# Performance work log

Measured on AMD Instinct MI355X. Metric: run time of the kernel, lower is better.

Reference implementation:

```python
import jax, jax.numpy as jnp
import numpy as np

B, T, I, H, O = 64, 256, 128, 512, 64
GRAD_CLIP = 5.0


def setup_inputs() -> dict:
    key = jax.random.key(0)
    ks = jax.random.split(key, 20)
    sH = 1.0 / np.sqrt(H)
    sI = 1.0 / np.sqrt(I)
    f32 = jnp.float32
    return {
        "x": jax.random.normal(ks[0], (B, T, I), f32),
        "y": jax.random.randint(ks[1], (B,), 0, O),
        "W1w": jax.random.normal(ks[2], (H, H), f32) * sH,
        "V1w": jax.random.normal(ks[3], (H, I), f32) * sI,
        "V1b": jnp.zeros((H,), f32),
        "W2w": jax.random.normal(ks[4], (H, H), f32) * sH,
        "W2b": jnp.zeros((H,), f32),
        "V2w": jax.random.normal(ks[5], (H, I), f32) * sI,
        "W3w": jax.random.normal(ks[6], (H, H), f32) * sH,
        "W3b": jnp.zeros((H,), f32),
        "V3w": jax.random.normal(ks[7], (H, I), f32) * sI,
        "Woutw": jax.random.normal(ks[8], (O, H), f32) * sH,
        "Woutb": jnp.zeros((O,), f32),
        "BW1": jax.random.normal(ks[9], (O, H), f32) * sH,
        "BV1": jax.random.normal(ks[10], (O, H), f32) * sH,
        "BW2": jax.random.normal(ks[11], (O, H), f32) * sH,
        "BV2": jax.random.normal(ks[12], (O, H), f32) * sH,
        "BW3": jax.random.normal(ks[13], (O, H), f32) * sH,
        "BV3": jax.random.normal(ks[14], (O, H), f32) * sH,
    }


def reference(x, y, W1w, V1w, V1b, W2w, W2b, V2w, W3w, W3b, V3w,
              Woutw, Woutb, BW1, BV1, BW2, BV2, BW3, BV3):
    Bsz, Tlen, _ = x.shape
    Hd = W1w.shape[0]
    Od = Woutw.shape[0]
    h0 = jnp.zeros((Bsz, Hd), x.dtype)
    xt = jnp.swapaxes(x, 0, 1)  # [T, B, I]

    def step(h, xti):
        z = jax.nn.sigmoid(h @ W2w.T + W2b + xti @ V2w.T)
        r = jax.nn.sigmoid(h @ W3w.T + W3b + xti @ V3w.T)
        ht = jnp.tanh(xti @ V1w.T + V1b + (h * r) @ W1w.T)
        hn = (1.0 - z) * ht + z * h
        return hn, (r, z, ht, hn)

    hT, (rs, zs, hs, hid) = jax.lax.scan(step, h0, xt)  # each [T, B, H]
    output = jax.nn.softmax(hT @ Woutw.T + Woutb, axis=-1)
    error = output - jax.nn.one_hot(y, Od, dtype=output.dtype)

    BW1e, BV1e = error @ BW1, error @ BV1
    BW2e, BV2e = error @ BW2, error @ BV2
    BW3e, BV3e = error @ BW3, error @ BV3

    hiddens = jnp.concatenate([h0[None], hid], axis=0)  # [T+1, B, H]
    # Faithfully replicate torch's hiddens[t-1] list indexing: at t=0 this is
    # hiddens[-1], i.e. the FINAL hidden state (Python negative indexing).
    idx = (np.arange(Tlen) - 1) % (Tlen + 1)
    hprev = hiddens[idx]  # [T, B, H]

    rr = rs * (1.0 - rs)
    sz = 1.0 - zs
    dh = 1.0 - hs ** 2

    # z-gate terms (index 1) -- original code uses r*(1-r) here, replicated.
    zg = (hprev - hs) * rr
    zgV = zg * BV2e[None]
    zgW = zg * BW2e[None]
    dV1 = jnp.einsum('tbh,tbi->hi', zgV, xt) / Bsz
    dW1 = jnp.einsum('tbh,tbH->hH', zgW, hprev) / Bsz
    db1 = zgV.sum(0).mean(0)

    # r-gate terms (index 2)
    AV = ((BV3e[None] * sz * dh) @ W1w.T) * hprev * rr
    AW = ((BW3e[None] * sz * dh) @ W1w.T) * hprev * rr
    dV2 = jnp.einsum('tbh,tbi->hi', AV, xt) / Bsz
    dW2 = jnp.einsum('tbh,tbH->hH', AW, hprev) / Bsz
    db2 = AV.sum(0).mean(0)

    # h-gate terms (index 0)
    HV = ((BV1e[None] * sz) @ W1w.T) * dh
    HW = ((BW1e[None] * sz) @ W1w.T) * dh
    dV0 = jnp.einsum('tbh,tbi->hi', HV, xt) / Bsz
    dW0 = jnp.einsum('tbh,tbH->hH', HW, rs * hprev) / Bsz
    db0 = HV.sum(0).mean(0)

    def nc(g):
        g = g / jnp.linalg.norm(g)
        return jnp.clip(g, -GRAD_CLIP, GRAD_CLIP)

    return (output, hT,
            nc(dW0), nc(dW1), nc(dW2),
            nc(dV0), nc(dV1), nc(dV2),
            nc(db0), nc(db1), nc(db2),
            error)
```

## Files before the change

kernel.cpp:

```cpp
#include <hip/hip_runtime.h>
#include <hip/hip_bf16.h>

#define DI __device__ __forceinline__

typedef __bf16 bf16x8 __attribute__((ext_vector_type(8)));
typedef __bf16 bf16x4 __attribute__((ext_vector_type(4)));
typedef __bf16 bf16x2 __attribute__((ext_vector_type(2)));
typedef float  f32x4  __attribute__((ext_vector_type(4)));
typedef unsigned long long ull;

static constexpr int Bc = 64, Tc = 256, Ic = 128, Hc = 512, Oc = 64;
static constexpr int TBc = Tc * Bc;
static constexpr size_t THW = (size_t)TBc * Hc;

static constexpr size_t O_OUT = 0;
static constexpr size_t O_HT  = 4096;
static constexpr size_t O_DW0 = 36864;
static constexpr size_t O_DV0 = 823296;
static constexpr size_t O_DB0 = 1019904;
static constexpr size_t O_ERR = 1021440;

static constexpr size_t W_CTR  = 0;
static constexpr size_t W_SLOT = 1024;
static constexpr size_t W_DB   = 2048;
static constexpr size_t W_FLG  = 8192;
static constexpr size_t W_ERRW = 16384;
static constexpr size_t W_PROJ = 32768;
static constexpr size_t W_W1B  = 819200;
static constexpr size_t W_HX   = 1343488;
static constexpr size_t W_HRX  = 1474560;
static constexpr size_t W_XT   = 1605632;
static constexpr size_t W_HIST = 5799936;
static constexpr size_t W_PB   = 72908800;
static constexpr size_t W_NEED = W_PB + 100663296;


DI void st32_agent(float* p, float v) {
  __hip_atomic_store((unsigned int*)p, __float_as_uint(v),
                     __ATOMIC_RELAXED, __HIP_MEMORY_SCOPE_AGENT);
}
DI ull ld64_agent(const void* p) {
  return __hip_atomic_load((ull*)p, __ATOMIC_RELAXED, __HIP_MEMORY_SCOPE_AGENT);
}

DI void group_barrier(int* flags_g, int myslot, int bar, bool& dead) {
  __syncthreads();
  if (threadIdx.x == 0)
    __hip_atomic_store(&flags_g[myslot * 32], bar,
                       __ATOMIC_RELAXED, __HIP_MEMORY_SCOPE_AGENT);
  if (threadIdx.x < 64 && !dead) {
    const int l = threadIdx.x;
    int spins = 0;
    for (;;) {
      int v = bar;
      if (l < 16)
        v = __hip_atomic_load(&flags_g[l * 32],
                              __ATOMIC_RELAXED, __HIP_MEMORY_SCOPE_AGENT);
      if (__all(v >= bar)) break;
      __builtin_amdgcn_s_sleep(1);
      if (++spins > 4000000) { dead = true; break; }
    }
  }
  __syncthreads();
}

DI float hprev_at(const __bf16* __restrict__ h_h, int k, int col) {
  int t = k >> 6;
  if (t == 1) return 0.f;
  int row = (t == 0) ? (16320 + (k & 63)) : (k - 128);
  return (float)h_h[(size_t)row * 512 + col];
}


__global__ void kzero(float* __restrict__ p, int n) {
  int i = blockIdx.x * 256 + threadIdx.x;
  if (i < n) p[i] = 0.f;
}
__global__ void ksent(float* p, float v) { p[0] = v; }
__global__ void k0_cast(const float* __restrict__ s, __bf16* __restrict__ d, int n) {
  int i = blockIdx.x * 256 + threadIdx.x;
  if (i < n) d[i] = (__bf16)s[i];
}

__global__ __launch_bounds__(256)
void k1_xv(const float* __restrict__ x, const float* __restrict__ V1w,
           const float* __restrict__ V2w, const float* __restrict__ V3w,
           const float* __restrict__ V1b, const float* __restrict__ W2b,
           const float* __restrict__ W3b,
           float* __restrict__ xv1f, float* __restrict__ xv2f, float* __restrict__ xv3f)
{
  const int cb = blockIdx.x, t = blockIdx.y;
  const int g = cb >> 3, jblk = cb & 7;
  const float* Vg   = (g == 0) ? V1w : (g == 1) ? V2w : V3w;
  const float* bias = (g == 0) ? V1b : (g == 1) ? W2b : W3b;
  float* of = (g == 0) ? xv1f : (g == 1) ? xv2f : xv3f;
  __shared__ float As[64 * 69];
  __shared__ float Bs[64 * 69];
  const int tid = threadIdx.x;
  float acc[4][4] = {};
  const int m0 = (tid & 15) * 4, j0 = (tid >> 4) * 4;
  for (int kc = 0; kc < 2; ++kc) {
    __syncthreads();
    #pragma unroll
    for (int e = 0; e < 4; ++e) {
      int idx = tid + e * 256;
      int row = idx >> 4, c4 = (idx & 15) * 4;
      float4 v = *reinterpret_cast<const float4*>(&x[((size_t)row * 256 + t) * 128 + kc * 64 + c4]);
      As[row * 69 + c4 + 0] = v.x; As[row * 69 + c4 + 1] = v.y;
      As[row * 69 + c4 + 2] = v.z; As[row * 69 + c4 + 3] = v.w;
      float4 w = *reinterpret_cast<const float4*>(&Vg[(size_t)(jblk * 64 + row) * 128 + kc * 64 + c4]);
      Bs[row * 69 + c4 + 0] = w.x; Bs[row * 69 + c4 + 1] = w.y;
      Bs[row * 69 + c4 + 2] = w.z; Bs[row * 69 + c4 + 3] = w.w;
    }
    __syncthreads();
    for (int i = 0; i < 64; ++i) {
      float a[4], b[4];
      #pragma unroll
      for (int u = 0; u < 4; ++u) a[u] = As[(m0 + u) * 69 + i];
      #pragma unroll
      for (int u = 0; u < 4; ++u) b[u] = Bs[(j0 + u) * 69 + i];
      #pragma unroll
      for (int mi = 0; mi < 4; ++mi)
        #pragma unroll
        for (int ji = 0; ji < 4; ++ji) acc[mi][ji] += a[mi] * b[ji];
    }
  }
  #pragma unroll
  for (int ji = 0; ji < 4; ++ji) {
    int jg = jblk * 64 + j0 + ji;
    float bv = bias[jg];
    #pragma unroll
    for (int mi = 0; mi < 4; ++mi) {
      int b = m0 + mi;
      of[((size_t)t * 64 + b) * 512 + jg] = acc[mi][ji] + bv;
    }
  }
}

__global__ void e0_xt(const float* __restrict__ x, __bf16* __restrict__ XT)
{
  const int t = blockIdx.x;
  __shared__ __bf16 xs[64 * 132];
  const int tid = threadIdx.x;
  #pragma unroll
  for (int e = 0; e < 8; ++e) {
    int idx = tid + e * 256;
    int b = idx >> 5, c4 = (idx & 31) * 4;
    float4 v = *reinterpret_cast<const float4*>(&x[((size_t)b * 256 + t) * 128 + c4]);
    xs[b * 132 + c4 + 0] = (__bf16)v.x; xs[b * 132 + c4 + 1] = (__bf16)v.y;
    xs[b * 132 + c4 + 2] = (__bf16)v.z; xs[b * 132 + c4 + 3] = (__bf16)v.w;
  }
  __syncthreads();
  #pragma unroll
  for (int e = 0; e < 8; ++e) {
    int idx = tid + e * 256;
    int i = idx >> 4, b4 = (idx & 15) * 4;
    __bf16* d = &XT[(size_t)i * TBc + t * 64 + b4];
    d[0] = xs[(b4 + 0) * 132 + i];
    d[1] = xs[(b4 + 1) * 132 + i];
    d[2] = xs[(b4 + 2) * 132 + i];
    d[3] = xs[(b4 + 3) * 132 + i];
  }
}

__global__ __launch_bounds__(256, 1)
void k2_recur(const float* __restrict__ W1w, const float* __restrict__ W2w,
              const float* __restrict__ W3w,
              const float* __restrict__ xv1, const float* __restrict__ xv2,
              const float* __restrict__ xv3,
              __bf16* __restrict__ r_h, __bf16* __restrict__ z_h,
              __bf16* __restrict__ ht_h, __bf16* __restrict__ h_h,
              float* __restrict__ hx, float* __restrict__ hrx,
              int* __restrict__ flags, float* __restrict__ dout)
{
  const int g  = blockIdx.x >> 4;
  const int cw = blockIdx.x & 15;
  const int tid = threadIdx.x, lane = tid & 63, wv = tid >> 6;
  const int kh = wv & 1;
  const int ct = wv >> 1;
  const int q  = lane >> 4;
  const int colc = cw * 32 + ct * 16 + (lane & 15);
  const bool owner = (kh == 0);

  __shared__ __align__(16) __bf16 c0[8192];
  __shared__ __align__(16) __bf16 c1[8192];
  __shared__ __align__(16) __bf16 c2[8192];
  __shared__ float pbuf[128 * 8];

  bf16x8 w1c[3][8], w2c[3][8], w3c[3][8];
  #pragma unroll
  for (int kk2 = 0; kk2 < 8; ++kk2) {
    const int kb = (kh * 8 + kk2) * 32 + q * 8;
    #pragma unroll
    for (int j = 0; j < 8; ++j) {
      float w = W1w[(size_t)colc * 512 + kb + j];
      __bf16 a = (__bf16)w; float r1 = w - (float)a;
      __bf16 b = (__bf16)r1;
      w1c[0][kk2][j] = a; w1c[1][kk2][j] = b; w1c[2][kk2][j] = (__bf16)(r1 - (float)b);
      w = W2w[(size_t)colc * 512 + kb + j];
      a = (__bf16)w; r1 = w - (float)a; b = (__bf16)r1;
      w2c[0][kk2][j] = a; w2c[1][kk2][j] = b; w2c[2][kk2][j] = (__bf16)(r1 - (float)b);
      w = W3w[(size_t)colc * 512 + kb + j];
      a = (__bf16)w; r1 = w - (float)a; b = (__bf16)r1;
      w3c[0][kk2][j] = a; w3c[1][kk2][j] = b; w3c[2][kk2][j] = (__bf16)(r1 - (float)b);
    }
  }
  for (int i = tid; i < 8192; i += 256) {
    c0[i] = (__bf16)0.f; c1[i] = (__bf16)0.f; c2[i] = (__bf16)0.f;
  }
  __syncthreads();

  float hreg[4] = {0.f, 0.f, 0.f, 0.f};
  float* hx_g  = hx  + g * 8192;
  float* hrx_g = hrx + g * 8192;
  int* flags_g = flags + g * 16 * 32;
  const int fragbase = (colc >> 5) * 512 + (((colc >> 3) & 3) * 16 + q * 4) * 8 + (colc & 7);
  const int pb = (ct * 64 + lane) * 8;

  auto stage = [&](const float* __restrict__ srcf) {
    const ull* src = reinterpret_cast<const ull*>(srcf);
    ull u[16];
    #pragma unroll
    for (int j = 0; j < 16; ++j) u[j] = ld64_agent(src + j * 256 + tid);
    #pragma unroll
    for (int j = 0; j < 16; ++j) {
      float f0 = __uint_as_float((unsigned int)u[j]);
      float f1 = __uint_as_float((unsigned int)(u[j] >> 32));
      __bf16 a0 = (__bf16)f0; float r0 = f0 - (float)a0; __bf16 b0 = (__bf16)r0;
      __bf16 d0 = (__bf16)(r0 - (float)b0);
      __bf16 a1 = (__bf16)f1; float r1 = f1 - (float)a1; __bf16 b1 = (__bf16)r1;
      __bf16 d1 = (__bf16)(r1 - (float)b1);
      int o = (j * 256 + tid) * 2;
      bf16x2 v0; v0[0] = a0; v0[1] = a1;
      bf16x2 v1; v1[0] = b0; v1[1] = b1;
      bf16x2 v2; v2[0] = d0; v2[1] = d1;
      *reinterpret_cast<bf16x2*>(&c0[o]) = v0;
      *reinterpret_cast<bf16x2*>(&c1[o]) = v1;
      *reinterpret_cast<bf16x2*>(&c2[o]) = v2;
    }
  };

  bool dead = false;
  int bar = 0;
  #pragma unroll 1
  for (int t = 0; t < Tc; ++t) {
    const size_t rowb = ((size_t)t * 64 + g * 16 + q * 4) * 512 + colc;
    float xv1v[4], xv2v[4], xv3v[4];
    if (owner) {
      #pragma unroll
      for (int i = 0; i < 4; ++i) {
        size_t o = rowb + (size_t)i * 512;
        xv1v[i] = xv1[o]; xv2v[i] = xv2[o]; xv3v[i] = xv3[o];
      }
    }
    f32x4 a2 = {0.f,0.f,0.f,0.f}, a3 = {0.f,0.f,0.f,0.f};
    #pragma unroll
    for (int kk2 = 0; kk2 < 8; ++kk2) {
      const int idx = (kh * 8 + kk2) * 512 + lane * 8;
      bf16x8 h0 = *reinterpret_cast<const bf16x8*>(&c0[idx]);
      bf16x8 h1 = *reinterpret_cast<const bf16x8*>(&c1[idx]);
      bf16x8 h2 = *reinterpret_cast<const bf16x8*>(&c2[idx]);
      a2 = __builtin_amdgcn_mfma_f32_16x16x32_bf16(h0, w2c[0][kk2], a2, 0, 0, 0);
      a2 = __builtin_amdgcn_mfma_f32_16x16x32_bf16(h1, w2c[0][kk2], a2, 0, 0, 0);
      a2 = __builtin_amdgcn_mfma_f32_16x16x32_bf16(h0, w2c[1][kk2], a2, 0, 0, 0);
      a2 = __builtin_amdgcn_mfma_f32_16x16x32_bf16(h2, w2c[0][kk2], a2, 0, 0, 0);
      a2 = __builtin_amdgcn_mfma_f32_16x16x32_bf16(h1, w2c[1][kk2], a2, 0, 0, 0);
      a2 = __builtin_amdgcn_mfma_f32_16x16x32_bf16(h0, w2c[2][kk2], a2, 0, 0, 0);
      a3 = __builtin_amdgcn_mfma_f32_16x16x32_bf16(h0, w3c[0][kk2], a3, 0, 0, 0);
      a3 = __builtin_amdgcn_mfma_f32_16x16x32_bf16(h1, w3c[0][kk2], a3, 0, 0, 0);
      a3 = __builtin_amdgcn_mfma_f32_16x16x32_bf16(h0, w3c[1][kk2], a3, 0, 0, 0);
      a3 = __builtin_amdgcn_mfma_f32_16x16x32_bf16(h2, w3c[0][kk2], a3, 0, 0, 0);
      a3 = __builtin_amdgcn_mfma_f32_16x16x32_bf16(h1, w3c[1][kk2], a3, 0, 0, 0);
      a3 = __builtin_amdgcn_mfma_f32_16x16x32_bf16(h0, w3c[2][kk2], a3, 0, 0, 0);
    }
    if (!owner) {
      #pragma unroll
      for (int i = 0; i < 4; ++i) { pbuf[pb + i] = a2[i]; pbuf[pb + 4 + i] = a3[i]; }
    }
    __syncthreads();
    float zz[4], rr4[4];
    if (owner) {
      #pragma unroll
      for (int i = 0; i < 4; ++i) {
        float s2 = a2[i] + pbuf[pb + i]     + xv2v[i];
        float s3 = a3[i] + pbuf[pb + 4 + i] + xv3v[i];
        zz[i]  = 1.f / (1.f + expf(-s2));
        rr4[i] = 1.f / (1.f + expf(-s3));
        st32_agent(&hrx_g[fragbase + i * 8], hreg[i] * rr4[i]);
      }
      #pragma unroll
      for (int i = 0; i < 4; ++i) {
        z_h[rowb + (size_t)i * 512] = (__bf16)zz[i];
        r_h[rowb + (size_t)i * 512] = (__bf16)rr4[i];
      }
    }
    ++bar; group_barrier(flags_g, cw, bar, dead);
    stage(hrx_g);
    __syncthreads();
    f32x4 a1 = {0.f,0.f,0.f,0.f};
    #pragma unroll
    for (int kk2 = 0; kk2 < 8; ++kk2) {
      const int idx = (kh * 8 + kk2) * 512 + lane * 8;
      bf16x8 h0 = *reinterpret_cast<const bf16x8*>(&c0[idx]);
      bf16x8 h1 = *reinterpret_cast<const bf16x8*>(&c1[idx]);
      bf16x8 h2 = *reinterpret_cast<const bf16x8*>(&c2[idx]);
      a1 = __builtin_amdgcn_mfma_f32_16x16x32_bf16(h0, w1c[0][kk2], a1, 0, 0, 0);
      a1 = __builtin_amdgcn_mfma_f32_16x16x32_bf16(h1, w1c[0][kk2], a1, 0, 0, 0);
      a1 = __builtin_amdgcn_mfma_f32_16x16x32_bf16(h0, w1c[1][kk2], a1, 0, 0, 0);
      a1 = __builtin_amdgcn_mfma_f32_16x16x32_bf16(h2, w1c[0][kk2], a1, 0, 0, 0);
      a1 = __builtin_amdgcn_mfma_f32_16x16x32_bf16(h1, w1c[1][kk2], a1, 0, 0, 0);
      a1 = __builtin_amdgcn_mfma_f32_16x16x32_bf16(h0, w1c[2][kk2], a1, 0, 0, 0);
    }
    if (!owner) {
      #pragma unroll
      for (int i = 0; i < 4; ++i) pbuf[pb + i] = a1[i];
    }
    __syncthreads();
    if (owner) {
      float htv[4];
      #pragma unroll
      for (int i = 0; i < 4; ++i) {
        float pre = a1[i] + pbuf[pb + i] + xv1v[i];
        float ht = tanhf(pre);
        float hn = zz[i] * (hreg[i] - ht) + ht;
        htv[i] = ht;
        hreg[i] = hn;
        st32_agent(&hx_g[fragbase + i * 8], hn);
      }
      #pragma unroll
      for (int i = 0; i < 4; ++i) {
        ht_h[rowb + (size_t)i * 512] = (__bf16)htv[i];
        h_h[rowb + (size_t)i * 512]  = (__bf16)hreg[i];
      }
    }
    ++bar; group_barrier(flags_g, cw, bar, dead);
    stage(hx_g);
    __syncthreads();
  }
  if (owner) {
    #pragma unroll
    for (int i = 0; i < 4; ++i) {
      int b = g * 16 + q * 4 + i;
      dout[O_HT + (size_t)b * 512 + colc] = hreg[i];
    }
  }
}

__global__ void k3a_soft(const float* __restrict__ Woutw, const float* __restrict__ Woutb,
                         const int* __restrict__ y, float* __restrict__ dout,
                         float* __restrict__ errw)
{
  const int b = blockIdx.x, o = threadIdx.x;
  const float* hrow = dout + O_HT + (size_t)b * 512;
  float sv = Woutb[o];
  for (int k = 0; k < 512; ++k) sv += hrow[k] * Woutw[(size_t)o * 512 + k];
  float mx = sv;
  for (int off = 32; off; off >>= 1) mx = fmaxf(mx, __shfl_xor(mx, off, 64));
  float e = expf(sv - mx);
  float sum = e;
  for (int off = 32; off; off >>= 1) sum += __shfl_xor(sum, off, 64);
  float outp = e / sum;
  float errv = outp - ((y[b] == o) ? 1.f : 0.f);
  dout[O_OUT + b * 64 + o] = outp;
  dout[O_ERR + b * 64 + o] = errv;
  errw[b * 64 + o] = errv;
}

__global__ __launch_bounds__(256)
void k3b_proj(const float* __restrict__ err,
              const float* b0, const float* b1, const float* b2,
              const float* b3, const float* b4, const float* b5,
              float* __restrict__ proj)
{
  const int p = blockIdx.y;
  const int hb = blockIdx.x * 64;
  const float* BX = (p==0)?b0:(p==1)?b1:(p==2)?b2:(p==3)?b3:(p==4)?b4:b5;
  __shared__ float es[64 * 64];
  __shared__ float bs[64 * 65];
  for (int i = threadIdx.x; i < 4096; i += 256) es[i] = err[i];
  for (int i = threadIdx.x; i < 4096; i += 256) {
    int o = i >> 6, hh = i & 63;
    bs[o * 65 + hh] = BX[(size_t)o * 512 + hb + hh];
  }
  __syncthreads();
  for (int e = 0; e < 16; ++e) {
    int idx = threadIdx.x + e * 256;
    int b = idx >> 6, hh = idx & 63;
    float s = 0.f;
    for (int o = 0; o < 64; ++o) s += es[b * 64 + o] * bs[o * 65 + hh];
    proj[(size_t)p * 32768 + b * 512 + hb + hh] = s;
  }
}

__global__ __launch_bounds__(256)
void e1t(const __bf16* __restrict__ r_h, const __bf16* __restrict__ h_h,
         __bf16* __restrict__ HpT, __bf16* __restrict__ RsHpT)
{
  const int t = blockIdx.y, hb = blockIdx.x * 64;
  const int tid = threadIdx.x;
  __shared__ __bf16 tr[64 * 68];
  float hpv[16], rv[16];
  #pragma unroll
  for (int e = 0; e < 16; ++e) {
    int idx = tid + e * 256;
    int b = idx >> 6, hl = idx & 63;
    hpv[e] = hprev_at(h_h, t * 64 + b, hb + hl);
    rv[e]  = (float)r_h[((size_t)t * 64 + b) * 512 + hb + hl];
  }
  for (int rnd = 0; rnd < 2; ++rnd) {
    __syncthreads();
    #pragma unroll
    for (int e = 0; e < 16; ++e) {
      int idx = tid + e * 256;
      int b = idx >> 6, hl = idx & 63;
      tr[b * 68 + hl] = (__bf16)(rnd == 0 ? hpv[e] : rv[e] * hpv[e]);
    }
    __syncthreads();
    __bf16* dst = (rnd == 0) ? HpT : RsHpT;
    #pragma unroll
    for (int e = 0; e < 16; ++e) {
      int idx = tid + e * 256;
      int hl2 = idx >> 6, b2 = idx & 63;
      dst[(size_t)(hb + hl2) * TBc + t * 64 + b2] = tr[b2 * 68 + hl2];
    }
  }
}

__global__ __launch_bounds__(256)
void k4_pgemm(const __bf16* __restrict__ z_h, const __bf16* __restrict__ ht_h,
              const __bf16* __restrict__ r_h, const __bf16* __restrict__ h_h,
              const float* __restrict__ proj, const __bf16* __restrict__ W1b,
              __bf16* __restrict__ P)
{
  const int p = blockIdx.z;
  const int krow0 = blockIdx.x * 128;
  const int n0 = blockIdx.y * 128;
  const int pidx = (p == 0) ? 5 : (p == 1) ? 4 : (p == 2) ? 1 : 0;
  const float* pr = proj + (size_t)pidx * 32768;
  const int tid = threadIdx.x, lane = tid & 63, wv = tid >> 6, q = lane >> 4;
  const int wm = (wv & 1) * 64, wn = (wv >> 1) * 64;
  __shared__ __align__(16) __bf16 Al[128 * 40];
  __shared__ __align__(16) __bf16 Bl[128 * 40];
  f32x4 acc[4][4] = {};
  for (int kt = 0; kt < 16; ++kt) {
    const int h0 = kt * 32;
    __syncthreads();
    #pragma unroll
    for (int e = 0; e < 4; ++e) {
      int idx = tid + e * 256;
      int row = idx >> 3, h4 = (idx & 7) * 4;
      int kg = krow0 + row;
      bf16x4 zz = *reinterpret_cast<const bf16x4*>(&z_h[(size_t)kg * 512 + h0 + h4]);
      bf16x4 tt = *reinterpret_cast<const bf16x4*>(&ht_h[(size_t)kg * 512 + h0 + h4]);
      float4 pv = *reinterpret_cast<const float4*>(&pr[(size_t)(kg & 63) * 512 + h0 + h4]);
      float pvv[4] = {pv.x, pv.y, pv.z, pv.w};
      bf16x4 gv;
      #pragma unroll
      for (int j = 0; j < 4; ++j) {
        float sz = 1.f - (float)zz[j];
        float v = pvv[j] * sz;
        if (p < 2) { float h = (float)tt[j]; v *= (1.f - h * h); }
        gv[j] = (__bf16)v;
      }
      *reinterpret_cast<bf16x4*>(&Al[row * 40 + h4]) = gv;
      bf16x4 wv4 = *reinterpret_cast<const bf16x4*>(&W1b[(size_t)(n0 + row) * 512 + h0 + h4]);
      *reinterpret_cast<bf16x4*>(&Bl[row * 40 + h4]) = wv4;
    }
    __syncthreads();
    bf16x8 af[4], bfv[4];
    #pragma unroll
    for (int mi = 0; mi < 4; ++mi)
      af[mi] = *reinterpret_cast<const bf16x8*>(&Al[(wm + mi * 16 + (lane & 15)) * 40 + q * 8]);
    #pragma unroll
    for (int ni = 0; ni < 4; ++ni)
      bfv[ni] = *reinterpret_cast<const bf16x8*>(&Bl[(wn + ni * 16 + (lane & 15)) * 40 + q * 8]);
    #pragma unroll
    for (int mi = 0; mi < 4; ++mi)
      #pragma unroll
      for (int ni = 0; ni < 4; ++ni)
        acc[mi][ni] = __builtin_amdgcn_mfma_f32_16x16x32_bf16(af[mi], bfv[ni], acc[mi][ni], 0, 0, 0);
  }
  __bf16* Pp = P + (size_t)p * THW;
  #pragma unroll
  for (int mi = 0; mi < 4; ++mi) {
    const int kg = krow0 + wm + mi * 16 + q * 4;
    const int tt = kg >> 6;
    #pragma unroll
    for (int ni = 0; ni < 4; ++ni) {
      const int n = n0 + wn + ni * 16 + (lane & 15);
      union { __bf16 b[4]; uint2 u; } pk;
      #pragma unroll
      for (int i = 0; i < 4; ++i) {
        float mul;
        if (p < 2) {
          float r = (float)r_h[(size_t)(kg + i) * 512 + n];
          float hp = 0.f;
          if (tt != 1) {
            int kr = (tt == 0) ? (16320 + (kg & 63) + i) : (kg + i - 128);
            hp = (float)h_h[(size_t)kr * 512 + n];
          }
          mul = hp * r * (1.f - r);
        } else {
          float h = (float)ht_h[(size_t)(kg + i) * 512 + n];
          mul = 1.f - h * h;
        }
        pk.b[i] = (__bf16)(acc[mi][ni][i] * mul);
      }
      *reinterpret_cast<uint2*>(&Pp[(size_t)n * TBc + kg]) = pk.u;
    }
  }
}

__global__ __launch_bounds__(256)
void k5_grad(const __bf16* __restrict__ Ap, int amode, const __bf16* __restrict__ Bp,
             const __bf16* __restrict__ r_h, const __bf16* __restrict__ ht_h,
             const __bf16* __restrict__ h_h, const float* __restrict__ projA,
             float* __restrict__ out, int N, int klen, float scale)
{
  const int m0 = blockIdx.x * 128;
  const int n0 = blockIdx.y * 128;
  const int tid = threadIdx.x, lane = tid & 63, wv = tid >> 6, q = lane >> 4;
  const int wm = (wv & 1) * 64, wn = (wv >> 1) * 64;
  __shared__ __align__(16) __bf16 Al[128 * 72];
  __shared__ __align__(16) __bf16 Bl[128 * 72];
  f32x4 acc[4][4] = {};
  const int iters = klen >> 6;
  for (int kt = 0; kt < iters; ++kt) {
    const int kk0 = blockIdx.z * klen + kt * 64;
    __syncthreads();
    #pragma unroll
    for (int e = 0; e < 8; ++e) {
      int idx = tid + e * 256;
      int row = idx >> 4, c4 = (idx & 15) * 4;
      bf16x4 bv = *reinterpret_cast<const bf16x4*>(&Bp[(size_t)(n0 + row) * TBc + kk0 + c4]);
      *reinterpret_cast<bf16x4*>(&Bl[row * 72 + c4]) = bv;
    }
    if (amode == 0) {
      #pragma unroll
      for (int e = 0; e < 8; ++e) {
        int idx = tid + e * 256;
        int row = idx >> 4, c4 = (idx & 15) * 4;
        bf16x4 av = *reinterpret_cast<const bf16x4*>(&Ap[(size_t)(m0 + row) * TBc + kk0 + c4]);
        *reinterpret_cast<bf16x4*>(&Al[row * 72 + c4]) = av;
      }
    } else {
      #pragma unroll
      for (int e = 0; e < 8; ++e) {
        int idx = tid + e * 256;
        int kk = idx >> 5;
        int m4 = (idx & 31) * 4;
        int kg = kk0 + kk;
        int tt = kg >> 6;
        bf16x4 hs = *reinterpret_cast<const bf16x4*>(&ht_h[(size_t)kg * 512 + m0 + m4]);
        bf16x4 rv = *reinterpret_cast<const bf16x4*>(&r_h[(size_t)kg * 512 + m0 + m4]);
        float4 pv = *reinterpret_cast<const float4*>(&projA[(size_t)(kg & 63) * 512 + m0 + m4]);
        float pvv[4] = {pv.x, pv.y, pv.z, pv.w};
        float hpf[4] = {0.f, 0.f, 0.f, 0.f};
        if (tt != 1) {
          int kr = (tt == 0) ? (16320 + (kg & 63)) : (kg - 128);
          bf16x4 hp = *reinterpret_cast<const bf16x4*>(&h_h[(size_t)kr * 512 + m0 + m4]);
          #pragma unroll
          for (int j = 0; j < 4; ++j) hpf[j] = (float)hp[j];
        }
        #pragma unroll
        for (int j = 0; j < 4; ++j) {
          float r = (float)rv[j];
          float zg = (hpf[j] - (float)hs[j]) * r * (1.f - r) * pvv[j];
          Al[(m4 + j) * 72 + kk] = (__bf16)zg;
        }
      }
    }
    __syncthreads();
    #pragma unroll
    for (int ks = 0; ks < 2; ++ks) {
      bf16x8 af[4], bfv[4];
      #pragma unroll
      for (int mi = 0; mi < 4; ++mi)
        af[mi] = *reinterpret_cast<const bf16x8*>(&Al[(wm + mi * 16 + (lane & 15)) * 72 + ks * 32 + q * 8]);
      #pragma unroll
      for (int ni = 0; ni < 4; ++ni)
        bfv[ni] = *reinterpret_cast<const bf16x8*>(&Bl[(wn + ni * 16 + (lane & 15)) * 72 + ks * 32 + q * 8]);
      #pragma unroll
      for (int mi = 0; mi < 4; ++mi)
        #pragma unroll
        for (int ni = 0; ni < 4; ++ni)
          acc[mi][ni] = __builtin_amdgcn_mfma_f32_16x16x32_bf16(af[mi], bfv[ni], acc[mi][ni], 0, 0, 0);
    }
  }
  #pragma unroll
  for (int mi = 0; mi < 4; ++mi) {
    const int m = m0 + wm + mi * 16 + q * 4;
    #pragma unroll
    for (int ni = 0; ni < 4; ++ni) {
      const int n = n0 + wn + ni * 16 + (lane & 15);
      #pragma unroll
      for (int i = 0; i < 4; ++i)
        atomicAdd(&out[(size_t)(m + i) * N + n], acc[mi][ni][i] * scale);
    }
  }
}

__global__ void k_dbP(const __bf16* __restrict__ P, float* __restrict__ db)
{
  const __bf16* row = P + (size_t)blockIdx.x * TBc;
  float sv = 0.f;
  for (int i = threadIdx.x; i < TBc; i += 256) sv += (float)row[i];
  for (int off = 32; off; off >>= 1) sv += __shfl_xor(sv, off, 64);
  __shared__ float red[4];
  if ((threadIdx.x & 63) == 0) red[threadIdx.x >> 6] = sv;
  __syncthreads();
  if (threadIdx.x == 0)
    atomicAdd(&db[blockIdx.x], (red[0] + red[1] + red[2] + red[3]) * (1.f / 64.f));
}

__global__ void k_dbzg(const __bf16* __restrict__ r_h, const __bf16* __restrict__ ht_h,
                       const __bf16* __restrict__ h_h, const float* __restrict__ proj,
                       float* __restrict__ db)
{
  const int hb = blockIdx.x * 64;
  const int col = hb + (threadIdx.x & 63);
  const int part = threadIdx.x >> 6;
  const int kb = blockIdx.y * 1024;
  float sum = 0.f;
  for (int k = kb + part; k < kb + 1024; k += 4) {
    float hs = (float)ht_h[(size_t)k * 512 + col];
    float r  = (float)r_h[(size_t)k * 512 + col];
    float hp = hprev_at(h_h, k, col);
    float pv = proj[3 * 32768 + (size_t)(k & 63) * 512 + col];
    sum += (hp - hs) * r * (1.f - r) * pv;
  }
  __shared__ float sred[4][64];
  sred[part][threadIdx.x & 63] = sum;
  __syncthreads();
  if (threadIdx.x < 64)
    atomicAdd(&db[512 + hb + threadIdx.x],
              (sred[0][threadIdx.x] + sred[1][threadIdx.x] +
               sred[2][threadIdx.x] + sred[3][threadIdx.x]) * (1.f / 64.f));
}

__global__ void k6a_sumsq(const float* __restrict__ dout, const float* __restrict__ db,
                          float* __restrict__ slots)
{
  const int yy = blockIdx.y;
  const float* src; int count;
  if (yy < 3)      { src = dout + O_DW0 + (size_t)yy * 262144; count = 262144; }
  else if (yy < 6) { src = dout + O_DV0 + (size_t)(yy - 3) * 65536; count = 65536; }
  else             { src = db + (size_t)(yy - 6) * 512; count = 512; }
  int start = blockIdx.x * 4096;
  if (start >= count) return;
  int end = min(start + 4096, count);
  float sp = 0.f;
  for (int i = start + threadIdx.x; i < end; i += 256) { float v = src[i]; sp += v * v; }
  for (int off = 32; off; off >>= 1) sp += __shfl_xor(sp, off, 64);
  __shared__ float red[4];
  if ((threadIdx.x & 63) == 0) red[threadIdx.x >> 6] = sp;
  __syncthreads();
  if (threadIdx.x == 0) atomicAdd(&slots[yy], red[0] + red[1] + red[2] + red[3]);
}

__global__ void k6b_write(const float* __restrict__ db,
                          const float* __restrict__ slots, float* __restrict__ dout)
{
  const int yy = blockIdx.y;
  const float* src; int count; size_t oo;
  if (yy < 3)      { oo = O_DW0 + (size_t)yy * 262144; src = dout + oo; count = 262144; }
  else if (yy < 6) { oo = O_DV0 + (size_t)(yy - 3) * 65536; src = dout + oo; count = 65536; }
  else             { oo = O_DB0 + (size_t)(yy - 6) * 512; src = db + (size_t)(yy - 6) * 512; count = 512; }
  int start = blockIdx.x * 4096;
  if (start >= count) return;
  int end = min(start + 4096, count);
  float inv = 1.f / sqrtf(slots[yy]);
  for (int i = start + threadIdx.x; i < end; i += 256) {
    float v = src[i] * inv;
    dout[oo + i] = fminf(fmaxf(v, -5.f), 5.f);
  }
}

extern "C" void kernel_launch(void* const* d_in, const int* in_sizes, int n_in,
                              void* d_out, int out_size, void* d_ws, size_t ws_size,
                              hipStream_t stream)
{
  const float* x     = (const float*)d_in[0];
  const int*   y     = (const int*)d_in[1];
  const float* W1w   = (const float*)d_in[2];
  const float* V1w   = (const float*)d_in[3];
  const float* V1b   = (const float*)d_in[4];
  const float* W2w   = (const float*)d_in[5];
  const float* W2b   = (const float*)d_in[6];
  const float* V2w   = (const float*)d_in[7];
  const float* W3w   = (const float*)d_in[8];
  const float* W3b   = (const float*)d_in[9];
  const float* V3w   = (const float*)d_in[10];
  const float* Woutw = (const float*)d_in[11];
  const float* Woutb = (const float*)d_in[12];
  const float* BW1   = (const float*)d_in[13];
  const float* BV1   = (const float*)d_in[14];
  const float* BW2   = (const float*)d_in[15];
  const float* BV2   = (const float*)d_in[16];
  const float* BW3   = (const float*)d_in[17];
  const float* BV3   = (const float*)d_in[18];
  float* dout = (float*)d_out;
  char* ws = (char*)d_ws;

  if (ws_size < W_NEED) { ksent<<<1, 1, 0, stream>>>(dout, (float)ws_size); return; }

  float*  slots = (float*)(ws + W_SLOT);
  float*  dbr   = (float*)(ws + W_DB);
  int*    flg   = (int*)(ws + W_FLG);
  float*  errw  = (float*)(ws + W_ERRW);
  float*  proj  = (float*)(ws + W_PROJ);
  __bf16* W1b   = (__bf16*)(ws + W_W1B);
  float*  hx    = (float*)(ws + W_HX);
  float*  hrx   = (float*)(ws + W_HRX);
  __bf16* XT    = (__bf16*)(ws + W_XT);
  __bf16* r_h   = (__bf16*)(ws + W_HIST);
  __bf16* z_h   = (__bf16*)(ws + W_HIST + 16777216);
  __bf16* ht_h  = (__bf16*)(ws + W_HIST + 33554432);
  __bf16* h_h   = (__bf16*)(ws + W_HIST + 50331648);
  char*   PB    = ws + W_PB;

  float* xv1 = (float*)PB;
  float* xv2 = (float*)(PB + 33554432);
  float* xv3 = (float*)(PB + 67108864);
  __bf16* P     = (__bf16*)PB;
  __bf16* HpT   = (__bf16*)(PB + 67108864);
  __bf16* RsHpT = (__bf16*)(PB + 83886080);

  kzero<<<16, 256, 0, stream>>>((float*)ws, 4096);
  kzero<<<3840, 256, 0, stream>>>(dout + O_DW0, 983040);
  k0_cast<<<1024, 256, 0, stream>>>(W1w, W1b, 262144);
  k1_xv<<<dim3(24, 256), 256, 0, stream>>>(x, V1w, V2w, V3w, V1b, W2b, W3b, xv1, xv2, xv3);
  e0_xt<<<256, 256, 0, stream>>>(x, XT);
  k2_recur<<<64, 256, 0, stream>>>(W1w, W2w, W3w, xv1, xv2, xv3,
                                   r_h, z_h, ht_h, h_h, hx, hrx, flg, dout);
  k3a_soft<<<64, 64, 0, stream>>>(Woutw, Woutb, y, dout, errw);
  k3b_proj<<<dim3(8, 6), 256, 0, stream>>>(errw, BW1, BV1, BW2, BV2, BW3, BV3, proj);
  e1t<<<dim3(8, 256), 256, 0, stream>>>(r_h, h_h, HpT, RsHpT);
  k_dbzg<<<dim3(8, 16), 256, 0, stream>>>(r_h, ht_h, h_h, proj, dbr);

  k4_pgemm<<<dim3(128, 4, 4), 256, 0, stream>>>(z_h, ht_h, r_h, h_h, proj, W1b, P);
  const float sc = 1.f / 64.f;
  k5_grad<<<dim3(4, 4, 16), 256, 0, stream>>>(P + 3 * THW, 0, RsHpT, r_h, ht_h, h_h, proj,
                                              dout + O_DW0, 512, 1024, sc);
  k5_grad<<<dim3(4, 4, 16), 256, 0, stream>>>(nullptr, 1, HpT, r_h, ht_h, h_h, proj + 2 * 32768,
                                              dout + O_DW0 + 262144, 512, 1024, sc);
  k5_grad<<<dim3(4, 4, 16), 256, 0, stream>>>(P + 1 * THW, 0, HpT, r_h, ht_h, h_h, proj,
                                              dout + O_DW0 + 524288, 512, 1024, sc);
  k5_grad<<<dim3(4, 1, 16), 256, 0, stream>>>(P + 2 * THW, 0, XT, r_h, ht_h, h_h, proj,
                                              dout + O_DV0, 128, 1024, sc);
  k5_grad<<<dim3(4, 1, 16), 256, 0, stream>>>(nullptr, 1, XT, r_h, ht_h, h_h, proj + 3 * 32768,
                                              dout + O_DV0 + 65536, 128, 1024, sc);
  k5_grad<<<dim3(4, 1, 16), 256, 0, stream>>>(P + 0 * THW, 0, XT, r_h, ht_h, h_h, proj,
                                              dout + O_DV0 + 131072, 128, 1024, sc);
  k_dbP<<<512, 256, 0, stream>>>(P + 2 * THW, dbr);
  k_dbP<<<512, 256, 0, stream>>>(P + 0 * THW, dbr + 1024);
  k6a_sumsq<<<dim3(64, 9), 256, 0, stream>>>(dout, dbr, slots);
  k6b_write<<<dim3(64, 9), 256, 0, stream>>>(dbr, slots, dout);
}
```

Baseline: 2.747 ms.

## Split recurrence K-dimension across four waves and prefetch next-step inputs

The recurrent kernel grows from 256 to 512 threads, splitting the 512-long reduction across four waves per column tile instead of two, with partial sums combined through a larger shared buffer. Each wave also keeps two independent MFMA accumulators to shorten the dependency chain. The precomputed input projections for step t+1 are loaded one step early, and the bf16 history stores are moved after the group barrier so they leave the critical path. The cost is extra shared-memory reduction traffic and more threads taking part in each block-level sync per step.

```diff
diff --git a/kernel.cpp b/kernel.cpp
--- a/kernel.cpp
+++ b/kernel.cpp
@@ -163,7 +163,7 @@
   }
 }
 
-__global__ __launch_bounds__(256, 1)
+__global__ __launch_bounds__(512, 1)
 void k2_recur(const float* __restrict__ W1w, const float* __restrict__ W2w,
               const float* __restrict__ W3w,
               const float* __restrict__ xv1, const float* __restrict__ xv2,
@@ -176,21 +176,21 @@
   const int g  = blockIdx.x >> 4;
   const int cw = blockIdx.x & 15;
   const int tid = threadIdx.x, lane = tid & 63, wv = tid >> 6;
-  const int kh = wv & 1;
-  const int ct = wv >> 1;
+  const int ks = wv & 3;
+  const int ct = wv >> 2;
   const int q  = lane >> 4;
   const int colc = cw * 32 + ct * 16 + (lane & 15);
-  const bool owner = (kh == 0);
+  const bool owner = (ks == 0);
 
   __shared__ __align__(16) __bf16 c0[8192];
   __shared__ __align__(16) __bf16 c1[8192];
   __shared__ __align__(16) __bf16 c2[8192];
-  __shared__ float pbuf[128 * 8];
-
-  bf16x8 w1c[3][8], w2c[3][8], w3c[3][8];
+  __shared__ float pbuf[3 * 128 * 8];
+
+  bf16x8 w1c[3][4], w2c[3][4], w3c[3][4];
   #pragma unroll
-  for (int kk2 = 0; kk2 < 8; ++kk2) {
-    const int kb = (kh * 8 + kk2) * 32 + q * 8;
+  for (int kk2 = 0; kk2 < 4; ++kk2) {
+    const int kb = (ks * 4 + kk2) * 32 + q * 8;
     #pragma unroll
     for (int j = 0; j < 8; ++j) {
       float w = W1w[(size_t)colc * 512 + kb + j];
@@ -205,7 +205,7 @@
       w3c[0][kk2][j] = a; w3c[1][kk2][j] = b; w3c[2][kk2][j] = (__bf16)(r1 - (float)b);
     }
   }
-  for (int i = tid; i < 8192; i += 256) {
+  for (int i = tid; i < 8192; i += 512) {
     c0[i] = (__bf16)0.f; c1[i] = (__bf16)0.f; c2[i] = (__bf16)0.f;
   }
   __syncthreads();
@@ -219,18 +219,18 @@
 
   auto stage = [&](const float* __restrict__ srcf) {
     const ull* src = reinterpret_cast<const ull*>(srcf);
-    ull u[16];
-    #pragma unroll
-    for (int j = 0; j < 16; ++j) u[j] = ld64_agent(src + j * 256 + tid);
-    #pragma unroll
-    for (int j = 0; j < 16; ++j) {
+    ull u[8];
+    #pragma unroll
+    for (int j = 0; j < 8; ++j) u[j] = ld64_agent(src + j * 512 + tid);
+    #pragma unroll
+    for (int j = 0; j < 8; ++j) {
       float f0 = __uint_as_float((unsigned int)u[j]);
       float f1 = __uint_as_float((unsigned int)(u[j] >> 32));
       __bf16 a0 = (__bf16)f0; float r0 = f0 - (float)a0; __bf16 b0 = (__bf16)r0;
       __bf16 d0 = (__bf16)(r0 - (float)b0);
       __bf16 a1 = (__bf16)f1; float r1 = f1 - (float)a1; __bf16 b1 = (__bf16)r1;
       __bf16 d1 = (__bf16)(r1 - (float)b1);
-      int o = (j * 256 + tid) * 2;
+      int o = (j * 512 + tid) * 2;
       bf16x2 v0; v0[0] = a0; v0[1] = a1;
       bf16x2 v1; v1[0] = b0; v1[1] = b1;
       bf16x2 v2; v2[0] = d0; v2[1] = d1;
@@ -240,100 +240,128 @@
     }
   };
 
+  auto rowbase = [&](int t) -> size_t {
+    return ((size_t)t * 64 + g * 16 + q * 4) * 512 + colc;
+  };
+
   bool dead = false;
   int bar = 0;
+  float xv1v[4], xv2v[4], xv3v[4];
+  if (owner) {
+    size_t r0 = rowbase(0);
+    #pragma unroll
+    for (int i = 0; i < 4; ++i) {
+      size_t o = r0 + (size_t)i * 512;
+      xv1v[i] = xv1[o]; xv2v[i] = xv2[o]; xv3v[i] = xv3[o];
+    }
+  }
   #pragma unroll 1
   for (int t = 0; t < Tc; ++t) {
-    const size_t rowb = ((size_t)t * 64 + g * 16 + q * 4) * 512 + colc;
-    float xv1v[4], xv2v[4], xv3v[4];
-    if (owner) {
+    const size_t rowb = rowbase(t);
+    float xn1[4], xn2[4], xn3[4];
+    if (owner && t + 1 < Tc) {
+      size_t rn = rowbase(t + 1);
       #pragma unroll
       for (int i = 0; i < 4; ++i) {
-        size_t o = rowb + (size_t)i * 512;
-        xv1v[i] = xv1[o]; xv2v[i] = xv2[o]; xv3v[i] = xv3[o];
-      }
-    }
-    f32x4 a2 = {0.f,0.f,0.f,0.f}, a3 = {0.f,0.f,0.f,0.f};
-    #pragma unroll
-    for (int kk2 = 0; kk2 < 8; ++kk2) {
-      const int idx = (kh * 8 + kk2) * 512 + lane * 8;
+        size_t o = rn + (size_t)i * 512;
+        xn1[i] = xv1[o]; xn2[i] = xv2[o]; xn3[i] = xv3[o];
+      }
+    }
+    f32x4 a2a = {0.f,0.f,0.f,0.f}, a2b = {0.f,0.f,0.f,0.f};
+    f32x4 a3a = {0.f,0.f,0.f,0.f}, a3b = {0.f,0.f,0.f,0.f};
+    #pragma unroll
+    for (int kk2 = 0; kk2 < 4; ++kk2) {
+      const int idx = (ks * 4 + kk2) * 512 + lane * 8;
       bf16x8 h0 = *reinterpret_cast<const bf16x8*>(&c0[idx]);
       bf16x8 h1 = *reinterpret_cast<const bf16x8*>(&c1[idx]);
       bf16x8 h2 = *reinterpret_cast<const bf16x8*>(&c2[idx]);
-      a2 = __builtin_amdgcn_mfma_f32_16x16x32_bf16(h0, w2c[0][kk2], a2, 0, 0, 0);
-      a2 = __builtin_amdgcn_mfma_f32_16x16x32_bf16(h1, w2c[0][kk2], a2, 0, 0, 0);
-      a2 = __builtin_amdgcn_mfma_f32_16x16x32_bf16(h0, w2c[1][kk2], a2, 0, 0, 0);
-      a2 = __builtin_amdgcn_mfma_f32_16x16x32_bf16(h2, w2c[0][kk2], a2, 0, 0, 0);
-      a2 = __builtin_amdgcn_mfma_f32_16x16x32_bf16(h1, w2c[1][kk2], a2, 0, 0, 0);
-      a2 = __builtin_amdgcn_mfma_f32_16x16x32_bf16(h0, w2c[2][kk2], a2, 0, 0, 0);
-      a3 = __builtin_amdgcn_mfma_f32_16x16x32_bf16(h0, w3c[0][kk2], a3, 0, 0, 0);
-      a3 = __builtin_amdgcn_mfma_f32_16x16x32_bf16(h1, w3c[0][kk2], a3, 0, 0, 0);
-      a3 = __builtin_amdgcn_mfma_f32_16x16x32_bf16(h0, w3c[1][kk2], a3, 0, 0, 0);
-      a3 = __builtin_amdgcn_mfma_f32_16x16x32_bf16(h2, w3c[0][kk2], a3, 0, 0, 0);
-      a3 = __builtin_amdgcn_mfma_f32_16x16x32_bf16(h1, w3c[1][kk2], a3, 0, 0, 0);
-      a3 = __builtin_amdgcn_mfma_f32_16x16x32_bf16(h0, w3c[2][kk2], a3, 0, 0, 0);
+      a2a = __builtin_amdgcn_mfma_f32_16x16x32_bf16(h0, w2c[0][kk2], a2a, 0, 0, 0);
+      a2b = __builtin_amdgcn_mfma_f32_16x16x32_bf16(h1, w2c[0][kk2], a2b, 0, 0, 0);
+      a2a = __builtin_amdgcn_mfma_f32_16x16x32_bf16(h0, w2c[1][kk2], a2a, 0, 0, 0);
+      a2b = __builtin_amdgcn_mfma_f32_16x16x32_bf16(h2, w2c[0][kk2], a2b, 0, 0, 0);
+      a2a = __builtin_amdgcn_mfma_f32_16x16x32_bf16(h1, w2c[1][kk2], a2a, 0, 0, 0);
+      a2b = __builtin_amdgcn_mfma_f32_16x16x32_bf16(h0, w2c[2][kk2], a2b, 0, 0, 0);
+      a3a = __builtin_amdgcn_mfma_f32_16x16x32_bf16(h0, w3c[0][kk2], a3a, 0, 0, 0);
+      a3b = __builtin_amdgcn_mfma_f32_16x16x32_bf16(h1, w3c[0][kk2], a3b, 0, 0, 0);
+      a3a = __builtin_amdgcn_mfma_f32_16x16x32_bf16(h0, w3c[1][kk2], a3a, 0, 0, 0);
+      a3b = __builtin_amdgcn_mfma_f32_16x16x32_bf16(h2, w3c[0][kk2], a3b, 0, 0, 0);
+      a3a = __builtin_amdgcn_mfma_f32_16x16x32_bf16(h1, w3c[1][kk2], a3a, 0, 0, 0);
+      a3b = __builtin_amdgcn_mfma_f32_16x16x32_bf16(h0, w3c[2][kk2], a3b, 0, 0, 0);
     }
     if (!owner) {
       #pragma unroll
-      for (int i = 0; i < 4; ++i) { pbuf[pb + i] = a2[i]; pbuf[pb + 4 + i] = a3[i]; }
+      for (int i = 0; i < 4; ++i) {
+        pbuf[(ks - 1) * 1024 + pb + i]     = a2a[i] + a2b[i];
+        pbuf[(ks - 1) * 1024 + pb + 4 + i] = a3a[i] + a3b[i];
+      }
     }
     __syncthreads();
     float zz[4], rr4[4];
     if (owner) {
       #pragma unroll
       for (int i = 0; i < 4; ++i) {
-        float s2 = a2[i] + pbuf[pb + i]     + xv2v[i];
-        float s3 = a3[i] + pbuf[pb + 4 + i] + xv3v[i];
+        float s2 = a2a[i] + a2b[i] + pbuf[pb + i] + pbuf[1024 + pb + i]
+                 + pbuf[2048 + pb + i] + xv2v[i];
+        float s3 = a3a[i] + a3b[i] + pbuf[pb + 4 + i] + pbuf[1024 + pb + 4 + i]
+                 + pbuf[2048 + pb + 4 + i] + xv3v[i];
         zz[i]  = 1.f / (1.f + expf(-s2));
         rr4[i] = 1.f / (1.f + expf(-s3));
         st32_agent(&hrx_g[fragbase + i * 8], hreg[i] * rr4[i]);
       }
+    }
+    ++bar; group_barrier(flags_g, cw, bar, dead);
+    if (owner) {
       #pragma unroll
       for (int i = 0; i < 4; ++i) {
         z_h[rowb + (size_t)i * 512] = (__bf16)zz[i];
         r_h[rowb + (size_t)i * 512] = (__bf16)rr4[i];
       }
     }
-    ++bar; group_barrier(flags_g, cw, bar, dead);
     stage(hrx_g);
     __syncthreads();
-    f32x4 a1 = {0.f,0.f,0.f,0.f};
-    #pragma unroll
-    for (int kk2 = 0; kk2 < 8; ++kk2) {
-      const int idx = (kh * 8 + kk2) * 512 + lane * 8;
+    f32x4 a1a = {0.f,0.f,0.f,0.f}, a1b = {0.f,0.f,0.f,0.f};
+    #pragma unroll
+    for (int kk2 = 0; kk2 < 4; ++kk2) {
+      const int idx = (ks * 4 + kk2) * 512 + lane * 8;
       bf16x8 h0 = *reinterpret_cast<const bf16x8*>(&c0[idx]);
       bf16x8 h1 = *reinterpret_cast<const bf16x8*>(&c1[idx]);
       bf16x8 h2 = *reinterpret_cast<const bf16x8*>(&c2[idx]);
-      a1 = __builtin_amdgcn_mfma_f32_16x16x32_bf16(h0, w1c[0][kk2], a1, 0, 0, 0);
-      a1 = __builtin_amdgcn_mfma_f32_16x16x32_bf16(h1, w1c[0][kk2], a1, 0, 0, 0);
-      a1 = __builtin_amdgcn_mfma_f32_16x16x32_bf16(h0, w1c[1][kk2], a1, 0, 0, 0);
-      a1 = __builtin_amdgcn_mfma_f32_16x16x32_bf16(h2, w1c[0][kk2], a1, 0, 0, 0);
-      a1 = __builtin_amdgcn_mfma_f32_16x16x32_bf16(h1, w1c[1][kk2], a1, 0, 0, 0);
-      a1 = __builtin_amdgcn_mfma_f32_16x16x32_bf16(h0, w1c[2][kk2], a1, 0, 0, 0);
+      a1a = __builtin_amdgcn_mfma_f32_16x16x32_bf16(h0, w1c[0][kk2], a1a, 0, 0, 0);
+      a1b = __builtin_amdgcn_mfma_f32_16x16x32_bf16(h1, w1c[0][kk2], a1b, 0, 0, 0);
+      a1a = __builtin_amdgcn_mfma_f32_16x16x32_bf16(h0, w1c[1][kk2], a1a, 0, 0, 0);
+      a1b = __builtin_amdgcn_mfma_f32_16x16x32_bf16(h2, w1c[0][kk2], a1b, 0, 0, 0);
+      a1a = __builtin_amdgcn_mfma_f32_16x16x32_bf16(h1, w1c[1][kk2], a1a, 0, 0, 0);
+      a1b = __builtin_amdgcn_mfma_f32_16x16x32_bf16(h0, w1c[2][kk2], a1b, 0, 0, 0);
     }
     if (!owner) {
       #pragma unroll
-      for (int i = 0; i < 4; ++i) pbuf[pb + i] = a1[i];
-    }
-    __syncthreads();
+      for (int i = 0; i < 4; ++i)
+        pbuf[(ks - 1) * 1024 + pb + i] = a1a[i] + a1b[i];
+    }
+    __syncthreads();
+    float htv[4];
     if (owner) {
-      float htv[4];
       #pragma unroll
       for (int i = 0; i < 4; ++i) {
-        float pre = a1[i] + pbuf[pb + i] + xv1v[i];
+        float pre = a1a[i] + a1b[i] + pbuf[pb + i] + pbuf[1024 + pb + i]
+                  + pbuf[2048 + pb + i] + xv1v[i];
         float ht = tanhf(pre);
         float hn = zz[i] * (hreg[i] - ht) + ht;
         htv[i] = ht;
         hreg[i] = hn;
         st32_agent(&hx_g[fragbase + i * 8], hn);
       }
+    }
+    ++bar; group_barrier(flags_g, cw, bar, dead);
+    if (owner) {
       #pragma unroll
       for (int i = 0; i < 4; ++i) {
         ht_h[rowb + (size_t)i * 512] = (__bf16)htv[i];
         h_h[rowb + (size_t)i * 512]  = (__bf16)hreg[i];
       }
-    }
-    ++bar; group_barrier(flags_g, cw, bar, dead);
+      #pragma unroll
+      for (int i = 0; i < 4; ++i) { xv1v[i] = xn1[i]; xv2v[i] = xn2[i]; xv3v[i] = xn3[i]; }
+    }
     stage(hx_g);
     __syncthreads();
   }
@@ -731,7 +759,7 @@
   k0_cast<<<1024, 256, 0, stream>>>(W1w, W1b, 262144);
   k1_xv<<<dim3(24, 256), 256, 0, stream>>>(x, V1w, V2w, V3w, V1b, W2b, W3b, xv1, xv2, xv3);
   e0_xt<<<256, 256, 0, stream>>>(x, XT);
-  k2_recur<<<64, 256, 0, stream>>>(W1w, W2w, W3w, xv1, xv2, xv3,
+  k2_recur<<<64, 512, 0, stream>>>(W1w, W2w, W3w, xv1, xv2, xv3,
                                    r_h, z_h, ht_h, h_h, hx, hrx, flg, dout);
   k3a_soft<<<64, 64, 0, stream>>>(Woutw, Woutb, y, dout, errw);
   k3b_proj<<<dim3(8, 6), 256, 0, stream>>>(errw, BW1, BV1, BW2, BV2, BW3, BV3, proj);
```

Result: slower. 3.165 ms (+15.2%).
